# Performance work log

Measured on AMD Instinct MI355X. Metric: run time of the kernel, lower is better.

## Reference

```python
import jax, jax.numpy as jnp
import numpy as np

E, W, C, D, F = 8, 8, 1024, 512, 2048  # local experts, world_size, capacity, d_model, d_ff


def setup_inputs() -> dict:
    key = jax.random.key(0)
    k1, k2, k3 = jax.random.split(key, 3)
    x = jax.random.normal(k1, (E, W, C, D), dtype=jnp.float32)
    cap = jax.random.randint(jax.random.fold_in(key, 7), (E,), 0, C)
    wi = jax.random.normal(k2, (E, D, F), dtype=jnp.float32) * 0.02
    wo = jax.random.normal(k3, (E, F, D), dtype=jnp.float32) * 0.02
    return {
        "dispatched_hidden_states": x,
        "experts_capacity_usage": cap,
        "wi": wi,
        "wo": wo,
    }


def reference(dispatched_hidden_states, experts_capacity_usage, wi, wo):
    # LocalExperts (handle_by_capacity=False): each expert e applies its own
    # T5 FFN to its chunk x[e]; expressed as a grouped GEMM over the expert axis.
    h = jnp.einsum("ewcd,edf->ewcf", dispatched_hidden_states, wi)  # [E,W,C,F]
    h = jax.nn.relu(h)
    out = jnp.einsum("ewcf,efd->ewcd", h, wo)  # [E,W,C,D]
    return out
```

## Files before the change

### kernel.cpp

```cpp
#include <hip/hip_runtime.h>
#include <hip/hip_bf16.h>
#include <stdint.h>


#define E_N 8
#define W_N 8
#define C_N 1024
#define D_N 512
#define F_N 2048
#define ME  (W_N * C_N)

typedef __attribute__((ext_vector_type(4))) float f32x4;
typedef __attribute__((ext_vector_type(8))) short s16x8;

#define BAR()  __builtin_amdgcn_s_barrier()
#define SBAR() __builtin_amdgcn_sched_barrier(0)
#define LGKM0() do { asm volatile("s_waitcnt lgkmcnt(0)" ::: "memory"); SBAR(); } while (0)
#define VM8()   do { asm volatile("s_waitcnt vmcnt(8)"   ::: "memory"); SBAR(); } while (0)
#define VM0()   do { asm volatile("s_waitcnt vmcnt(0)"   ::: "memory"); SBAR(); } while (0)

__device__ __forceinline__ unsigned short f2bf(float f) {
  union { float f; unsigned int u; } v; v.f = f;
  unsigned int u = v.u + 0x7fffu + ((v.u >> 16) & 1u);
  return (unsigned short)(u >> 16);
}

__device__ __forceinline__ void gload_lds16(void* lds, const void* g) {
  __builtin_amdgcn_global_load_lds(
      (const __attribute__((address_space(1))) unsigned int*)g,
      (__attribute__((address_space(3))) unsigned int*)lds, 16, 0, 0);
}

__global__ __launch_bounds__(256)
void transpose_cvt(const float* __restrict__ in, unsigned short* __restrict__ out,
                   int R, int Ccols) {
  __shared__ unsigned short tile[64][65];
  const int e = blockIdx.z;
  const float* ip = in + (size_t)e * R * Ccols;
  unsigned short* op = out + (size_t)e * R * Ccols;
  const int c0 = blockIdx.x * 64, r0 = blockIdx.y * 64;
  const int t = threadIdx.x;
  const int cl = (t & 15) * 4, rw = t >> 4;
#pragma unroll
  for (int i = 0; i < 4; ++i) {
    int row = rw + i * 16;
    float4 v = *(const float4*)&ip[(size_t)(r0 + row) * Ccols + c0 + cl];
    tile[row][cl + 0] = f2bf(v.x);
    tile[row][cl + 1] = f2bf(v.y);
    tile[row][cl + 2] = f2bf(v.z);
    tile[row][cl + 3] = f2bf(v.w);
  }
  __syncthreads();
#pragma unroll
  for (int i = 0; i < 4; ++i) {
    int oc = rw + i * 16;
    ushort4 o;
    o.x = tile[cl + 0][oc];
    o.y = tile[cl + 1][oc];
    o.z = tile[cl + 2][oc];
    o.w = tile[cl + 3][oc];
    *(ushort4*)&op[(size_t)(c0 + oc) * R + r0 + cl] = o;
  }
}

__global__ __launch_bounds__(256)
void cvt_x_kernel(const float* __restrict__ in, unsigned short* __restrict__ out, size_t n) {
  size_t idx = ((size_t)blockIdx.x * 256 + threadIdx.x) * 8;
  const size_t stride = (size_t)gridDim.x * 256 * 8;
  for (; idx < n; idx += stride) {
    float4 a = *(const float4*)&in[idx];
    float4 b = *(const float4*)&in[idx + 4];
    union { s16x8 v; unsigned short u[8]; } p;
    p.u[0] = f2bf(a.x); p.u[1] = f2bf(a.y); p.u[2] = f2bf(a.z); p.u[3] = f2bf(a.w);
    p.u[4] = f2bf(b.x); p.u[5] = f2bf(b.y); p.u[6] = f2bf(b.z); p.u[7] = f2bf(b.w);
    *(s16x8*)&out[idx] = p.v;
  }
}

template<bool RELU_BF16_OUT>
__global__ __launch_bounds__(512, 2)
void gemm256(const unsigned short* __restrict__ Abase,
             const unsigned short* __restrict__ Btbase,
             void* __restrict__ Cv, int N, int K,
             size_t aStrideE, size_t bStrideE, size_t cStrideE) {
  extern __shared__ unsigned short lds[];
  unsigned char* ldsb = (unsigned char*)lds;
  const int e = blockIdx.z;
  const int m0 = blockIdx.x * 256;
  const int n0 = blockIdx.y * 256;
  const int tid  = threadIdx.x;
  const int lane = tid & 63;
  const int wave = tid >> 6;
  const int wm = wave >> 2;
  const int wn = wave & 3;
  const unsigned short* A  = Abase  + (size_t)e * aStrideE;
  const unsigned short* Bt = Btbase + (size_t)e * bStrideE;

  const int NK = K >> 6;
  const int NI = NK >> 1;

  const int rl = lane & 15;
  const int gb = lane >> 4;
  const int g16_0 = ((0 * 4 + gb) ^ (rl & 7)) * 16;
  const int g16_1 = ((1 * 4 + gb) ^ (rl & 7)) * 16;
  const int aBase0 = wm * 16384 + rl * 128;
  const int bBase0 = 32768 + (wn >> 1) * 16384 + ((wn & 1) * 64 + rl) * 128;

  int rOffA[2], rOffB[2];
#pragma unroll
  for (int o = 0; o < 2; ++o) {
    int G = o * 512 + tid;
    int r = G >> 3;
    int gl = (G & 7) ^ (r & 7);
    rOffA[o] = (m0 + r) * K + gl * 8;
    rOffB[o] = (n0 + r) * K + gl * 8;
  }
  auto stageA = [&](int kt, int h) {
    const int buf = kt & 1;
#pragma unroll
    for (int o = 0; o < 2; ++o)
      gload_lds16(ldsb + buf * 65536 + h * 16384 + o * 8192 + wave * 1024,
                  A + rOffA[o] + h * 128 * K + kt * 64);
  };
  auto stageB = [&](int kt, int h) {
    const int buf = kt & 1;
#pragma unroll
    for (int o = 0; o < 2; ++o)
      gload_lds16(ldsb + buf * 65536 + 32768 + h * 16384 + o * 8192 + wave * 1024,
                  Bt + rOffB[o] + h * 128 * K + kt * 64);
  };

  f32x4 acc[8][4] = {};

  stageB(0, 0); stageB(0, 1); stageA(0, 0); stageA(0, 1);
  stageB(1, 0); stageB(1, 1); stageA(1, 0); stageA(1, 1);
  VM8();
  BAR();

  auto run_ktile = [&](int buf, int ktN, bool more, bool needDrain) {
    const int bufOff = buf * 65536;
    s16x8 afr[4][2], b01[2][2], b23[2][2];
#pragma unroll
    for (int mi = 0; mi < 4; ++mi) {
      afr[mi][0] = *(const s16x8*)(ldsb + bufOff + aBase0 + mi * 2048 + g16_0);
      afr[mi][1] = *(const s16x8*)(ldsb + bufOff + aBase0 + mi * 2048 + g16_1);
    }
#pragma unroll
    for (int ni = 0; ni < 2; ++ni) {
      b01[ni][0] = *(const s16x8*)(ldsb + bufOff + bBase0 + ni * 2048 + g16_0);
      b01[ni][1] = *(const s16x8*)(ldsb + bufOff + bBase0 + ni * 2048 + g16_1);
    }
    BAR(); LGKM0();
    __builtin_amdgcn_s_setprio(1);
#pragma unroll
    for (int mi = 0; mi < 4; ++mi)
#pragma unroll
      for (int ni = 0; ni < 2; ++ni) {
        acc[mi][ni] = __builtin_amdgcn_mfma_f32_16x16x32_bf16(afr[mi][0], b01[ni][0], acc[mi][ni], 0, 0, 0);
        acc[mi][ni] = __builtin_amdgcn_mfma_f32_16x16x32_bf16(afr[mi][1], b01[ni][1], acc[mi][ni], 0, 0, 0);
      }
    __builtin_amdgcn_s_setprio(0);
    BAR();
#pragma unroll
    for (int ni = 0; ni < 2; ++ni) {
      b23[ni][0] = *(const s16x8*)(ldsb + bufOff + bBase0 + (2 + ni) * 2048 + g16_0);
      b23[ni][1] = *(const s16x8*)(ldsb + bufOff + bBase0 + (2 + ni) * 2048 + g16_1);
    }
    BAR(); LGKM0();
    __builtin_amdgcn_s_setprio(1);
#pragma unroll
    for (int mi = 0; mi < 4; ++mi)
#pragma unroll
      for (int ni = 0; ni < 2; ++ni) {
        acc[mi][2 + ni] = __builtin_amdgcn_mfma_f32_16x16x32_bf16(afr[mi][0], b23[ni][0], acc[mi][2 + ni], 0, 0, 0);
        acc[mi][2 + ni] = __builtin_amdgcn_mfma_f32_16x16x32_bf16(afr[mi][1], b23[ni][1], acc[mi][2 + ni], 0, 0, 0);
      }
    __builtin_amdgcn_s_setprio(0);
    BAR();
#pragma unroll
    for (int mi = 0; mi < 4; ++mi) {
      afr[mi][0] = *(const s16x8*)(ldsb + bufOff + aBase0 + (4 + mi) * 2048 + g16_0);
      afr[mi][1] = *(const s16x8*)(ldsb + bufOff + aBase0 + (4 + mi) * 2048 + g16_1);
    }
    if (more) { stageB(ktN, 0); stageB(ktN, 1); }
    BAR(); LGKM0();
    __builtin_amdgcn_s_setprio(1);
#pragma unroll
    for (int mi = 0; mi < 4; ++mi)
#pragma unroll
      for (int ni = 0; ni < 2; ++ni) {
        acc[4 + mi][2 + ni] = __builtin_amdgcn_mfma_f32_16x16x32_bf16(afr[mi][0], b23[ni][0], acc[4 + mi][2 + ni], 0, 0, 0);
        acc[4 + mi][2 + ni] = __builtin_amdgcn_mfma_f32_16x16x32_bf16(afr[mi][1], b23[ni][1], acc[4 + mi][2 + ni], 0, 0, 0);
      }
    __builtin_amdgcn_s_setprio(0);
    BAR();
    if (more) { stageA(ktN, 0); stageA(ktN, 1); }
    BAR();
    __builtin_amdgcn_s_setprio(1);
#pragma unroll
    for (int mi = 0; mi < 4; ++mi)
#pragma unroll
      for (int ni = 0; ni < 2; ++ni) {
        acc[4 + mi][ni] = __builtin_amdgcn_mfma_f32_16x16x32_bf16(afr[mi][0], b01[ni][0], acc[4 + mi][ni], 0, 0, 0);
        acc[4 + mi][ni] = __builtin_amdgcn_mfma_f32_16x16x32_bf16(afr[mi][1], b01[ni][1], acc[4 + mi][ni], 0, 0, 0);
      }
    __builtin_amdgcn_s_setprio(0);
    if (more) { VM8(); } else if (needDrain) { VM0(); }
    BAR();
  };

  for (int i = 0; i < NI; ++i) {
    const bool more = (i + 1 < NI);
    run_ktile(0, 2 * i + 2, more, true);
    run_ktile(1, 2 * i + 3, more, false);
  }

  const int rq = (lane >> 4) * 4;
  const int cq = lane & 15;
  if (RELU_BF16_OUT) {
    unsigned short* Cb = (unsigned short*)Cv + (size_t)e * cStrideE;
#pragma unroll
    for (int mi = 0; mi < 8; ++mi)
#pragma unroll
      for (int ni = 0; ni < 4; ++ni) {
        int row0 = m0 + wm * 128 + mi * 16 + rq;
        int col  = n0 + wn * 64 + ni * 16 + cq;
#pragma unroll
        for (int r = 0; r < 4; ++r) {
          float v = acc[mi][ni][r];
          v = v > 0.f ? v : 0.f;
          Cb[(size_t)(row0 + r) * N + col] = f2bf(v);
        }
      }
  } else {
    float* Cf = (float*)Cv + (size_t)e * cStrideE;
#pragma unroll
    for (int mi = 0; mi < 8; ++mi)
#pragma unroll
      for (int ni = 0; ni < 4; ++ni) {
        int row0 = m0 + wm * 128 + mi * 16 + rq;
        int col  = n0 + wn * 64 + ni * 16 + cq;
#pragma unroll
        for (int r = 0; r < 4; ++r)
          Cf[(size_t)(row0 + r) * N + col] = acc[mi][ni][r];
      }
  }
}

__global__ __launch_bounds__(256)
void fused_naive(const float* __restrict__ x, const float* __restrict__ wi,
                 const float* __restrict__ wo, float* __restrict__ out) {
  __shared__ float xs[D_N];
  __shared__ float hs[F_N];
  const size_t row = blockIdx.x;
  const int e = (int)(row / (W_N * C_N));
  const float* xr = x + row * D_N;
  const float* wie = wi + (size_t)e * D_N * F_N;
  const float* woe = wo + (size_t)e * F_N * D_N;
  const int t = threadIdx.x;
  for (int d = t; d < D_N; d += 256) xs[d] = xr[d];
  __syncthreads();
  for (int f = t; f < F_N; f += 256) {
    float a = 0.f;
    for (int d = 0; d < D_N; ++d) a += xs[d] * wie[(size_t)d * F_N + f];
    hs[f] = a > 0.f ? a : 0.f;
  }
  __syncthreads();
  float* orow = out + row * D_N;
  for (int d = t; d < D_N; d += 256) {
    float a = 0.f;
    for (int f = 0; f < F_N; ++f) a += hs[f] * woe[(size_t)f * D_N + d];
    orow[d] = a;
  }
}

extern "C" void kernel_launch(void* const* d_in, const int* in_sizes, int n_in,
                              void* d_out, int out_size, void* d_ws, size_t ws_size,
                              hipStream_t stream) {
  const float* x  = (const float*)d_in[0];
  const float* wi = (const float*)d_in[2];
  const float* wo = (const float*)d_in[3];
  float* out = (float*)d_out;

  const size_t WT   = (size_t)E_N * D_N * F_N;
  unsigned short* wiT = (unsigned short*)d_ws;
  unsigned short* woT = wiT + WT;
  unsigned short* P   = woT + WT;
  const size_t baseB = 2 * WT * 2;
  const size_t XB_B  = (size_t)E_N * ME * D_N * 2;
  const size_t HF_B  = (size_t)E_N * ME * F_N * 2;

  const dim3 blk(256);
  if (ws_size >= baseB + XB_B + HF_B) {
    hipFuncSetAttribute(reinterpret_cast<const void*>(gemm256<true>),
                        hipFuncAttributeMaxDynamicSharedMemorySize, 131072);
    hipFuncSetAttribute(reinterpret_cast<const void*>(gemm256<false>),
                        hipFuncAttributeMaxDynamicSharedMemorySize, 131072);
    transpose_cvt<<<dim3(F_N / 64, D_N / 64, E_N), blk, 0, stream>>>(wi, wiT, D_N, F_N);
    transpose_cvt<<<dim3(D_N / 64, F_N / 64, E_N), blk, 0, stream>>>(wo, woT, F_N, D_N);
    unsigned short* xb = P;
    unsigned short* h  = P + XB_B / 2;
    cvt_x_kernel<<<2048, blk, 0, stream>>>(x, xb, (size_t)E_N * ME * D_N);
    gemm256<true><<<dim3(ME / 256, F_N / 256, E_N), dim3(512), 131072, stream>>>(
        xb, wiT, h, F_N, D_N, (size_t)ME * D_N, (size_t)F_N * D_N, (size_t)ME * F_N);
    gemm256<false><<<dim3(ME / 256, D_N / 256, E_N), dim3(512), 131072, stream>>>(
        h, woT, out, D_N, F_N, (size_t)ME * F_N, (size_t)D_N * F_N, (size_t)ME * D_N);
  } else {
    fused_naive<<<dim3(E_N * W_N * C_N), blk, 0, stream>>>(x, wi, wo, out);
  }
}
```

Baseline: 400.6 us.

## Make GEMM kernels persistent over N tiles with continuous cross-tile prefetch

Both grouped GEMMs now launch 256 blocks, one per (expert, 256-row M tile). Each block walks all N tiles in sequence, running a single flattened k-loop in which the next tile's loads are staged while the current tile finishes. This removes the pipeline ramp-up and drain at every tile boundary and keeps the A tile hot in cache. The cost is that all 256 blocks must fit in one wave on the GPU; if they do not, load balance suffers. The epilogue stores now sit inside the main loop and can stall the MFMA pipeline.

```diff
diff --git a/kernel.cpp b/kernel.cpp
--- a/kernel.cpp
+++ b/kernel.cpp
@@ -79,15 +79,15 @@
 
 template<bool RELU_BF16_OUT>
 __global__ __launch_bounds__(512, 2)
-void gemm256(const unsigned short* __restrict__ Abase,
-             const unsigned short* __restrict__ Btbase,
-             void* __restrict__ Cv, int N, int K,
-             size_t aStrideE, size_t bStrideE, size_t cStrideE) {
+void gemm256p(const unsigned short* __restrict__ Abase,
+              const unsigned short* __restrict__ Btbase,
+              void* __restrict__ Cv, int N, int K, int nTN,
+              size_t aStrideE, size_t bStrideE, size_t cStrideE) {
   extern __shared__ unsigned short lds[];
   unsigned char* ldsb = (unsigned char*)lds;
-  const int e = blockIdx.z;
-  const int m0 = blockIdx.x * 256;
-  const int n0 = blockIdx.y * 256;
+  const int blk = blockIdx.x;
+  const int e  = blk & 7;
+  const int m0 = (blk >> 3) * 256;
   const int tid  = threadIdx.x;
   const int lane = tid & 63;
   const int wave = tid >> 6;
@@ -97,7 +97,8 @@
   const unsigned short* Bt = Btbase + (size_t)e * bStrideE;
 
   const int NK = K >> 6;
-  const int NI = NK >> 1;
+  const int kshift = __builtin_ctz(NK);
+  const int total = nTN * NK;
 
   const int rl = lane & 15;
   const int gb = lane >> 4;
@@ -106,144 +107,154 @@
   const int aBase0 = wm * 16384 + rl * 128;
   const int bBase0 = 32768 + (wn >> 1) * 16384 + ((wn & 1) * 64 + rl) * 128;
 
-  int rOffA[2], rOffB[2];
+  int rOffA[2], rB0[2];
 #pragma unroll
   for (int o = 0; o < 2; ++o) {
     int G = o * 512 + tid;
     int r = G >> 3;
     int gl = (G & 7) ^ (r & 7);
     rOffA[o] = (m0 + r) * K + gl * 8;
-    rOffB[o] = (n0 + r) * K + gl * 8;
-  }
-  auto stageA = [&](int kt, int h) {
-    const int buf = kt & 1;
+    rB0[o]   = r * K + gl * 8;
+  }
+  auto stageA = [&](int g, int h) {
+    const int ktl = g & (NK - 1);
+    const int buf = g & 1;
 #pragma unroll
     for (int o = 0; o < 2; ++o)
       gload_lds16(ldsb + buf * 65536 + h * 16384 + o * 8192 + wave * 1024,
-                  A + rOffA[o] + h * 128 * K + kt * 64);
+                  A + rOffA[o] + h * 128 * K + ktl * 64);
   };
-  auto stageB = [&](int kt, int h) {
-    const int buf = kt & 1;
+  auto stageB = [&](int g, int h) {
+    const int ktl = g & (NK - 1);
+    const int buf = g & 1;
+    const unsigned short* Bn = Bt + (size_t)((g >> kshift) * 256) * K;
 #pragma unroll
     for (int o = 0; o < 2; ++o)
       gload_lds16(ldsb + buf * 65536 + 32768 + h * 16384 + o * 8192 + wave * 1024,
-                  Bt + rOffB[o] + h * 128 * K + kt * 64);
+                  Bn + rB0[o] + h * 128 * K + ktl * 64);
   };
 
   f32x4 acc[8][4] = {};
+
+  auto run_ktile = [&](int buf, int gN, bool more, bool needDrain) {
+    const int bufOff = buf * 65536;
+    s16x8 afr[4][2], b01[2][2], b23[2][2];
+#pragma unroll
+    for (int mi = 0; mi < 4; ++mi) {
+      afr[mi][0] = *(const s16x8*)(ldsb + bufOff + aBase0 + mi * 2048 + g16_0);
+      afr[mi][1] = *(const s16x8*)(ldsb + bufOff + aBase0 + mi * 2048 + g16_1);
+    }
+#pragma unroll
+    for (int ni = 0; ni < 2; ++ni) {
+      b01[ni][0] = *(const s16x8*)(ldsb + bufOff + bBase0 + ni * 2048 + g16_0);
+      b01[ni][1] = *(const s16x8*)(ldsb + bufOff + bBase0 + ni * 2048 + g16_1);
+    }
+    BAR(); LGKM0();
+    __builtin_amdgcn_s_setprio(1);
+#pragma unroll
+    for (int mi = 0; mi < 4; ++mi)
+#pragma unroll
+      for (int ni = 0; ni < 2; ++ni) {
+        acc[mi][ni] = __builtin_amdgcn_mfma_f32_16x16x32_bf16(afr[mi][0], b01[ni][0], acc[mi][ni], 0, 0, 0);
+        acc[mi][ni] = __builtin_amdgcn_mfma_f32_16x16x32_bf16(afr[mi][1], b01[ni][1], acc[mi][ni], 0, 0, 0);
+      }
+    __builtin_amdgcn_s_setprio(0);
+    BAR();
+#pragma unroll
+    for (int ni = 0; ni < 2; ++ni) {
+      b23[ni][0] = *(const s16x8*)(ldsb + bufOff + bBase0 + (2 + ni) * 2048 + g16_0);
+      b23[ni][1] = *(const s16x8*)(ldsb + bufOff + bBase0 + (2 + ni) * 2048 + g16_1);
+    }
+    BAR(); LGKM0();
+    __builtin_amdgcn_s_setprio(1);
+#pragma unroll
+    for (int mi = 0; mi < 4; ++mi)
+#pragma unroll
+      for (int ni = 0; ni < 2; ++ni) {
+        acc[mi][2 + ni] = __builtin_amdgcn_mfma_f32_16x16x32_bf16(afr[mi][0], b23[ni][0], acc[mi][2 + ni], 0, 0, 0);
+        acc[mi][2 + ni] = __builtin_amdgcn_mfma_f32_16x16x32_bf16(afr[mi][1], b23[ni][1], acc[mi][2 + ni], 0, 0, 0);
+      }
+    __builtin_amdgcn_s_setprio(0);
+    BAR();
+#pragma unroll
+    for (int mi = 0; mi < 4; ++mi) {
+      afr[mi][0] = *(const s16x8*)(ldsb + bufOff + aBase0 + (4 + mi) * 2048 + g16_0);
+      afr[mi][1] = *(const s16x8*)(ldsb + bufOff + aBase0 + (4 + mi) * 2048 + g16_1);
+    }
+    if (more) { stageB(gN, 0); stageB(gN, 1); }
+    BAR(); LGKM0();
+    __builtin_amdgcn_s_setprio(1);
+#pragma unroll
+    for (int mi = 0; mi < 4; ++mi)
+#pragma unroll
+      for (int ni = 0; ni < 2; ++ni) {
+        acc[4 + mi][2 + ni] = __builtin_amdgcn_mfma_f32_16x16x32_bf16(afr[mi][0], b23[ni][0], acc[4 + mi][2 + ni], 0, 0, 0);
+        acc[4 + mi][2 + ni] = __builtin_amdgcn_mfma_f32_16x16x32_bf16(afr[mi][1], b23[ni][1], acc[4 + mi][2 + ni], 0, 0, 0);
+      }
+    __builtin_amdgcn_s_setprio(0);
+    BAR();
+    if (more) { stageA(gN, 0); stageA(gN, 1); }
+    BAR();
+    __builtin_amdgcn_s_setprio(1);
+#pragma unroll
+    for (int mi = 0; mi < 4; ++mi)
+#pragma unroll
+      for (int ni = 0; ni < 2; ++ni) {
+        acc[4 + mi][ni] = __builtin_amdgcn_mfma_f32_16x16x32_bf16(afr[mi][0], b01[ni][0], acc[4 + mi][ni], 0, 0, 0);
+        acc[4 + mi][ni] = __builtin_amdgcn_mfma_f32_16x16x32_bf16(afr[mi][1], b01[ni][1], acc[4 + mi][ni], 0, 0, 0);
+      }
+    __builtin_amdgcn_s_setprio(0);
+    if (more) { VM8(); } else if (needDrain) { VM0(); }
+    BAR();
+  };
 
   stageB(0, 0); stageB(0, 1); stageA(0, 0); stageA(0, 1);
   stageB(1, 0); stageB(1, 1); stageA(1, 0); stageA(1, 1);
   VM8();
   BAR();
 
-  auto run_ktile = [&](int buf, int ktN, bool more, bool needDrain) {
-    const int bufOff = buf * 65536;
-    s16x8 afr[4][2], b01[2][2], b23[2][2];
-#pragma unroll
-    for (int mi = 0; mi < 4; ++mi) {
-      afr[mi][0] = *(const s16x8*)(ldsb + bufOff + aBase0 + mi * 2048 + g16_0);
-      afr[mi][1] = *(const s16x8*)(ldsb + bufOff + aBase0 + mi * 2048 + g16_1);
-    }
-#pragma unroll
-    for (int ni = 0; ni < 2; ++ni) {
-      b01[ni][0] = *(const s16x8*)(ldsb + bufOff + bBase0 + ni * 2048 + g16_0);
-      b01[ni][1] = *(const s16x8*)(ldsb + bufOff + bBase0 + ni * 2048 + g16_1);
-    }
-    BAR(); LGKM0();
-    __builtin_amdgcn_s_setprio(1);
-#pragma unroll
-    for (int mi = 0; mi < 4; ++mi)
-#pragma unroll
-      for (int ni = 0; ni < 2; ++ni) {
-        acc[mi][ni] = __builtin_amdgcn_mfma_f32_16x16x32_bf16(afr[mi][0], b01[ni][0], acc[mi][ni], 0, 0, 0);
-        acc[mi][ni] = __builtin_amdgcn_mfma_f32_16x16x32_bf16(afr[mi][1], b01[ni][1], acc[mi][ni], 0, 0, 0);
-      }
-    __builtin_amdgcn_s_setprio(0);
-    BAR();
-#pragma unroll
-    for (int ni = 0; ni < 2; ++ni) {
-      b23[ni][0] = *(const s16x8*)(ldsb + bufOff + bBase0 + (2 + ni) * 2048 + g16_0);
-      b23[ni][1] = *(const s16x8*)(ldsb + bufOff + bBase0 + (2 + ni) * 2048 + g16_1);
-    }
-    BAR(); LGKM0();
-    __builtin_amdgcn_s_setprio(1);
-#pragma unroll
-    for (int mi = 0; mi < 4; ++mi)
-#pragma unroll
-      for (int ni = 0; ni < 2; ++ni) {
-        acc[mi][2 + ni] = __builtin_amdgcn_mfma_f32_16x16x32_bf16(afr[mi][0], b23[ni][0], acc[mi][2 + ni], 0, 0, 0);
-        acc[mi][2 + ni] = __builtin_amdgcn_mfma_f32_16x16x32_bf16(afr[mi][1], b23[ni][1], acc[mi][2 + ni], 0, 0, 0);
-      }
-    __builtin_amdgcn_s_setprio(0);
-    BAR();
-#pragma unroll
-    for (int mi = 0; mi < 4; ++mi) {
-      afr[mi][0] = *(const s16x8*)(ldsb + bufOff + aBase0 + (4 + mi) * 2048 + g16_0);
-      afr[mi][1] = *(const s16x8*)(ldsb + bufOff + aBase0 + (4 + mi) * 2048 + g16_1);
-    }
-    if (more) { stageB(ktN, 0); stageB(ktN, 1); }
-    BAR(); LGKM0();
-    __builtin_amdgcn_s_setprio(1);
-#pragma unroll
-    for (int mi = 0; mi < 4; ++mi)
-#pragma unroll
-      for (int ni = 0; ni < 2; ++ni) {
-        acc[4 + mi][2 + ni] = __builtin_amdgcn_mfma_f32_16x16x32_bf16(afr[mi][0], b23[ni][0], acc[4 + mi][2 + ni], 0, 0, 0);
-        acc[4 + mi][2 + ni] = __builtin_amdgcn_mfma_f32_16x16x32_bf16(afr[mi][1], b23[ni][1], acc[4 + mi][2 + ni], 0, 0, 0);
-      }
-    __builtin_amdgcn_s_setprio(0);
-    BAR();
-    if (more) { stageA(ktN, 0); stageA(ktN, 1); }
-    BAR();
-    __builtin_amdgcn_s_setprio(1);
-#pragma unroll
-    for (int mi = 0; mi < 4; ++mi)
-#pragma unroll
-      for (int ni = 0; ni < 2; ++ni) {
-        acc[4 + mi][ni] = __builtin_amdgcn_mfma_f32_16x16x32_bf16(afr[mi][0], b01[ni][0], acc[4 + mi][ni], 0, 0, 0);
-        acc[4 + mi][ni] = __builtin_amdgcn_mfma_f32_16x16x32_bf16(afr[mi][1], b01[ni][1], acc[4 + mi][ni], 0, 0, 0);
-      }
-    __builtin_amdgcn_s_setprio(0);
-    if (more) { VM8(); } else if (needDrain) { VM0(); }
-    BAR();
-  };
-
-  for (int i = 0; i < NI; ++i) {
-    const bool more = (i + 1 < NI);
-    run_ktile(0, 2 * i + 2, more, true);
-    run_ktile(1, 2 * i + 3, more, false);
-  }
-
   const int rq = (lane >> 4) * 4;
   const int cq = lane & 15;
-  if (RELU_BF16_OUT) {
-    unsigned short* Cb = (unsigned short*)Cv + (size_t)e * cStrideE;
-#pragma unroll
-    for (int mi = 0; mi < 8; ++mi)
-#pragma unroll
-      for (int ni = 0; ni < 4; ++ni) {
-        int row0 = m0 + wm * 128 + mi * 16 + rq;
-        int col  = n0 + wn * 64 + ni * 16 + cq;
-#pragma unroll
-        for (int r = 0; r < 4; ++r) {
-          float v = acc[mi][ni][r];
-          v = v > 0.f ? v : 0.f;
-          Cb[(size_t)(row0 + r) * N + col] = f2bf(v);
-        }
-      }
-  } else {
-    float* Cf = (float*)Cv + (size_t)e * cStrideE;
-#pragma unroll
-    for (int mi = 0; mi < 8; ++mi)
-#pragma unroll
-      for (int ni = 0; ni < 4; ++ni) {
-        int row0 = m0 + wm * 128 + mi * 16 + rq;
-        int col  = n0 + wn * 64 + ni * 16 + cq;
-#pragma unroll
-        for (int r = 0; r < 4; ++r)
-          Cf[(size_t)(row0 + r) * N + col] = acc[mi][ni][r];
-      }
+
+  for (int g = 0; g < total; g += 2) {
+    run_ktile(0, g + 2, (g + 2 < total), true);
+    run_ktile(1, g + 3, (g + 3 < total), false);
+    if (((g + 2) & (NK - 1)) == 0) {
+      const int n0 = (g >> kshift) * 256;
+      if (RELU_BF16_OUT) {
+        unsigned short* Cb = (unsigned short*)Cv + (size_t)e * cStrideE;
+#pragma unroll
+        for (int mi = 0; mi < 8; ++mi)
+#pragma unroll
+          for (int ni = 0; ni < 4; ++ni) {
+            int row0 = m0 + wm * 128 + mi * 16 + rq;
+            int col  = n0 + wn * 64 + ni * 16 + cq;
+#pragma unroll
+            for (int r = 0; r < 4; ++r) {
+              float v = acc[mi][ni][r];
+              v = v > 0.f ? v : 0.f;
+              Cb[(size_t)(row0 + r) * N + col] = f2bf(v);
+            }
+          }
+      } else {
+        float* Cf = (float*)Cv + (size_t)e * cStrideE;
+#pragma unroll
+        for (int mi = 0; mi < 8; ++mi)
+#pragma unroll
+          for (int ni = 0; ni < 4; ++ni) {
+            int row0 = m0 + wm * 128 + mi * 16 + rq;
+            int col  = n0 + wn * 64 + ni * 16 + cq;
+#pragma unroll
+            for (int r = 0; r < 4; ++r)
+              Cf[(size_t)(row0 + r) * N + col] = acc[mi][ni][r];
+          }
+      }
+#pragma unroll
+      for (int mi = 0; mi < 8; ++mi)
+#pragma unroll
+        for (int ni = 0; ni < 4; ++ni)
+          acc[mi][ni] = (f32x4){0.f, 0.f, 0.f, 0.f};
+    }
   }
 }
 
@@ -292,19 +303,21 @@
 
   const dim3 blk(256);
   if (ws_size >= baseB + XB_B + HF_B) {
-    hipFuncSetAttribute(reinterpret_cast<const void*>(gemm256<true>),
+    hipFuncSetAttribute(reinterpret_cast<const void*>(gemm256p<true>),
                         hipFuncAttributeMaxDynamicSharedMemorySize, 131072);
-    hipFuncSetAttribute(reinterpret_cast<const void*>(gemm256<false>),
+    hipFuncSetAttribute(reinterpret_cast<const void*>(gemm256p<false>),
                         hipFuncAttributeMaxDynamicSharedMemorySize, 131072);
     transpose_cvt<<<dim3(F_N / 64, D_N / 64, E_N), blk, 0, stream>>>(wi, wiT, D_N, F_N);
     transpose_cvt<<<dim3(D_N / 64, F_N / 64, E_N), blk, 0, stream>>>(wo, woT, F_N, D_N);
     unsigned short* xb = P;
     unsigned short* h  = P + XB_B / 2;
     cvt_x_kernel<<<2048, blk, 0, stream>>>(x, xb, (size_t)E_N * ME * D_N);
-    gemm256<true><<<dim3(ME / 256, F_N / 256, E_N), dim3(512), 131072, stream>>>(
-        xb, wiT, h, F_N, D_N, (size_t)ME * D_N, (size_t)F_N * D_N, (size_t)ME * F_N);
-    gemm256<false><<<dim3(ME / 256, D_N / 256, E_N), dim3(512), 131072, stream>>>(
-        h, woT, out, D_N, F_N, (size_t)ME * F_N, (size_t)D_N * F_N, (size_t)ME * D_N);
+    gemm256p<true><<<dim3(256), dim3(512), 131072, stream>>>(
+        xb, wiT, h, F_N, D_N, F_N / 256,
+        (size_t)ME * D_N, (size_t)F_N * D_N, (size_t)ME * F_N);
+    gemm256p<false><<<dim3(256), dim3(512), 131072, stream>>>(
+        h, woT, out, D_N, F_N, D_N / 256,
+        (size_t)ME * F_N, (size_t)D_N * F_N, (size_t)ME * D_N);
   } else {
     fused_naive<<<dim3(E_N * W_N * C_N), blk, 0, stream>>>(x, wi, wo, out);
   }
```

New measurement: 506.0 us. +26.3%, slower.
